# Kernel tuning notes

Hardware: AMD Instinct MI355X
Metric: run time of the kernel (lower is better)

The kernel has to match this reference:

```python
import jax, jax.numpy as jnp
import numpy as np

def setup_inputs() -> dict:
    key = jax.random.key(0)
    k1, k2 = jax.random.split(key)
    N, M, D = 4096, 4096, 1024
    set1 = jax.random.normal(k1, (N, D), dtype=jnp.float32)
    set2 = jax.random.normal(k2, (M, D), dtype=jnp.float32)
    return {"set1": set1, "set2": set2}

def _l2_dist(x, y):
    # mean over D of squared differences, computed via the expanded GEMM form
    D = x.shape[-1]
    x2 = jnp.sum(x * x, axis=-1)          # [N]
    y2 = jnp.sum(y * y, axis=-1)          # [M]
    xy = jnp.einsum('nd,md->nm', x, y)    # [N, M]
    return (x2[:, None] - 2.0 * xy + y2[None, :]) / D

def reference(set1, set2):
    dist = _l2_dist(set1, set2)                 # [N, M]
    t1 = jnp.mean(jnp.min(dist, axis=1))        # nearest set2 point per set1 point
    t2 = jnp.mean(jnp.min(dist, axis=0))        # nearest set1 point per set2 point
    return (t1 + t2) * 0.5
```

## Files before the change

### kernel.cpp

```cpp
#include <hip/hip_runtime.h>
#include <hip/hip_bf16.h>
#include <stdint.h>


#define NPTS 4096
#define MPTS 4096
#define DDIM 1024

typedef __attribute__((ext_vector_type(8))) short bf16x8;
typedef __attribute__((ext_vector_type(4))) float f32x4;

__device__ __forceinline__ unsigned short f2bf(float f) {
    unsigned int u = __float_as_uint(f);
    unsigned int r = 0x7FFFu + ((u >> 16) & 1u);
    return (unsigned short)((u + r) >> 16);
}

__device__ __forceinline__ void gl_lds16(const void* g, void* l) {
    __builtin_amdgcn_global_load_lds(
        (const __attribute__((address_space(1))) unsigned int*)g,
        (__attribute__((address_space(3))) unsigned int*)l, 16, 0, 0);
}

__global__ __launch_bounds__(256) void prepass_kernel(
    const float* __restrict__ s1, const float* __restrict__ s2,
    unsigned short* __restrict__ b1, unsigned short* __restrict__ b2,
    float* __restrict__ norms, unsigned int* __restrict__ mins) {
    const int row = blockIdx.x * 4 + (threadIdx.x >> 6);
    const int lane = threadIdx.x & 63;
    const float* src;
    unsigned short* dst;
    if (row < NPTS) { src = s1 + (size_t)row * DDIM; dst = b1 + (size_t)row * DDIM; }
    else            { src = s2 + (size_t)(row - NPTS) * DDIM; dst = b2 + (size_t)(row - NPTS) * DDIM; }
    float sq = 0.f;
    #pragma unroll
    for (int i = 0; i < 4; ++i) {
        float4 v = ((const float4*)src)[lane + i * 64];
        sq += v.x * v.x + v.y * v.y + v.z * v.z + v.w * v.w;
        ushort4 o;
        o.x = f2bf(v.x); o.y = f2bf(v.y); o.z = f2bf(v.z); o.w = f2bf(v.w);
        ((ushort4*)dst)[lane + i * 64] = o;
    }
    #pragma unroll
    for (int off = 32; off; off >>= 1) sq += __shfl_down(sq, off, 64);
    if (lane == 0) { norms[row] = sq; mins[row] = 0x7f7f7f7fu; }
}


#define STAGE_H(ldsBase, gRowBase, kcol) do {                                   \
    gl_lds16((gRowBase) + (size_t)(wave * 8 + srow) * DDIM + (kcol) + schoff,   \
             ldsb + (ldsBase) + wave * 1024);                                   \
    gl_lds16((gRowBase) + (size_t)(64 + wave * 8 + srow) * DDIM + (kcol) + schoff, \
             ldsb + (ldsBase) + 8192 + wave * 1024);                            \
} while (0)

#define RD_A(CURB, aq) do {                                                     \
    _Pragma("unroll")                                                           \
    for (int fl_ = 0; fl_ < 4; ++fl_) {                                         \
        const int row_ = wr * 128 + (aq) * 64 + fl_ * 16 + r0;                  \
        af[fl_][0] = *(const bf16x8*)(ldsb + (CURB) + row_ * 128 + ch0);        \
        af[fl_][1] = *(const bf16x8*)(ldsb + (CURB) + row_ * 128 + ch1);        \
    }                                                                           \
} while (0)

#define RD_B(CURB, bq, dst) do {                                                \
    _Pragma("unroll")                                                           \
    for (int fj_ = 0; fj_ < 2; ++fj_) {                                         \
        const int col_ = wc * 64 + (bq) * 32 + fj_ * 16 + r0;                   \
        dst[fj_][0] = *(const bf16x8*)(ldsb + (CURB) + 32768 + col_ * 128 + ch0); \
        dst[fj_][1] = *(const bf16x8*)(ldsb + (CURB) + 32768 + col_ * 128 + ch1); \
    }                                                                           \
} while (0)

#define MFMA_Q(aq, bq, BF)                                                      \
    _Pragma("unroll")                                                           \
    for (int fl_ = 0; fl_ < 4; ++fl_) {                                         \
        _Pragma("unroll")                                                       \
        for (int fj_ = 0; fj_ < 2; ++fj_) {                                     \
            acc[(aq) * 4 + fl_][(bq) * 2 + fj_] =                               \
                __builtin_amdgcn_mfma_f32_16x16x32_bf16(af[fl_][0], BF[fj_][0], \
                    acc[(aq) * 4 + fl_][(bq) * 2 + fj_], 0, 0, 0);              \
            acc[(aq) * 4 + fl_][(bq) * 2 + fj_] =                               \
                __builtin_amdgcn_mfma_f32_16x16x32_bf16(af[fl_][1], BF[fj_][1], \
                    acc[(aq) * 4 + fl_][(bq) * 2 + fj_], 0, 0, 0);              \
        }                                                                       \
    }

#define BARRIER_MFMA(aq, bq, BF, WAITSTMT) do {                                 \
    __builtin_amdgcn_s_barrier();                                               \
    asm volatile("s_waitcnt lgkmcnt(0)" ::: "memory");                          \
    __builtin_amdgcn_sched_barrier(0);                                          \
    __builtin_amdgcn_s_setprio(1);                                              \
    MFMA_Q(aq, bq, BF);                                                         \
    __builtin_amdgcn_s_setprio(0);                                              \
    WAITSTMT;                                                                   \
    __builtin_amdgcn_s_barrier();                                               \
} while (0)

#define TILE(t, CURB, NXTB) do {                                                \
    const int kN1_ = ((t) + 1) * 64, kN2_ = ((t) + 2) * 64;                     \
                                                 \
    RD_A(CURB, 0); RD_B(CURB, 0, bf0);                                          \
    if ((t) + 1 < 16) STAGE_H((NXTB) + 49152, Bb + 128 * DDIM, kN1_);           \
    BARRIER_MFMA(0, 0, bf0, );                                                  \
                                                 \
    RD_B(CURB, 1, bf1);                                                         \
    if ((t) + 1 < 16) STAGE_H((NXTB) + 16384, Ab + 128 * DDIM, kN1_);           \
    BARRIER_MFMA(0, 1, bf1, );                                                  \
                                                 \
    RD_A(CURB, 1);                                                              \
    if ((t) + 2 < 16) STAGE_H((CURB) + 32768, Bb, kN2_);                        \
    BARRIER_MFMA(1, 1, bf1, );                                                  \
                                   \
    if ((t) + 2 < 16) STAGE_H((CURB) + 0, Ab, kN2_);                            \
    BARRIER_MFMA(1, 0, bf0,                                                     \
        if ((t) < 14) { asm volatile("s_waitcnt vmcnt(4)" ::: "memory"); }      \
        else if ((t) == 14) { asm volatile("s_waitcnt vmcnt(0)" ::: "memory"); });\
} while (0)

__global__ __launch_bounds__(512, 2) void cham_gemm_kernel(
    const unsigned short* __restrict__ A,
    const unsigned short* __restrict__ B,
    const float* __restrict__ x2, const float* __restrict__ y2,
    unsigned int* __restrict__ rowmin, unsigned int* __restrict__ colmin) {
    __shared__ __align__(16) char lds[131072];
    char* ldsb = lds;

    const int bi = blockIdx.x & 15;
    const int bj = blockIdx.x >> 4;
    const int tid = threadIdx.x;
    const int wave = tid >> 6;
    const int lane = tid & 63;
    const int wr = wave >> 2;
    const int wc = wave & 3;
    const int r0 = lane & 15;
    const int q = lane >> 4;

    const int ch0 = ((q ^ (r0 & 7)) << 4);
    const int ch1 = (((4 + q) ^ (r0 & 7)) << 4);

    const int srow = lane >> 3;
    const int schoff = (((lane & 7) ^ srow) * 8);

    const unsigned short* Ab = A + (size_t)(bi * 256) * DDIM;
    const unsigned short* Bb = B + (size_t)(bj * 256) * DDIM;

    f32x4 acc[8][4];
    #pragma unroll
    for (int i = 0; i < 8; ++i)
        #pragma unroll
        for (int j = 0; j < 4; ++j)
            acc[i][j] = (f32x4){0.f, 0.f, 0.f, 0.f};

    bf16x8 af[4][2], bf0[2][2], bf1[2][2];

    STAGE_H(0 + 32768, Bb, 0);
    STAGE_H(0 + 0, Ab, 0);
    STAGE_H(0 + 49152, Bb + 128 * DDIM, 0);
    STAGE_H(0 + 16384, Ab + 128 * DDIM, 0);
    STAGE_H(65536 + 32768, Bb, 64);
    STAGE_H(65536 + 0, Ab, 64);
    asm volatile("s_waitcnt vmcnt(4)" ::: "memory");
    __builtin_amdgcn_s_barrier();

    for (int tt = 0; tt < 8; ++tt) {
        const int te = 2 * tt, to = 2 * tt + 1;
        TILE(te, 0, 65536);
        TILE(to, 65536, 0);
    }

    const float invD = 1.0f / (float)DDIM;
    const int nb = bi * 256 + wr * 128;
    const int mb = bj * 256 + wc * 64;

    float y2v[4];
    #pragma unroll
    for (int fj = 0; fj < 4; ++fj)
        y2v[fj] = y2[mb + (fj >> 1) * 32 + (fj & 1) * 16 + r0];

    float cv[4];
    #pragma unroll
    for (int fj = 0; fj < 4; ++fj) cv[fj] = 3.0e38f;

    #pragma unroll
    for (int fi = 0; fi < 8; ++fi) {
        #pragma unroll
        for (int rg = 0; rg < 4; ++rg) {
            const int n = nb + fi * 16 + q * 4 + rg;
            const float x2v = x2[n];
            float rv = 3.0e38f;
            #pragma unroll
            for (int fj = 0; fj < 4; ++fj) {
                float d = (x2v + y2v[fj] - 2.0f * acc[fi][fj][rg]) * invD;
                rv = fminf(rv, d);
                cv[fj] = fminf(cv[fj], d);
            }
            rv = fminf(rv, __shfl_xor(rv, 1, 64));
            rv = fminf(rv, __shfl_xor(rv, 2, 64));
            rv = fminf(rv, __shfl_xor(rv, 4, 64));
            rv = fminf(rv, __shfl_xor(rv, 8, 64));
            if (r0 == 0) atomicMin(&rowmin[n], __float_as_uint(rv));
        }
    }

    #pragma unroll
    for (int fj = 0; fj < 4; ++fj) {
        float v = cv[fj];
        v = fminf(v, __shfl_xor(v, 16, 64));
        v = fminf(v, __shfl_xor(v, 32, 64));
        if (lane < 16)
            atomicMin(&colmin[mb + (fj >> 1) * 32 + (fj & 1) * 16 + lane],
                      __float_as_uint(v));
    }
}

__global__ __launch_bounds__(1024) void finredux_kernel(
    const unsigned int* __restrict__ mins , float* __restrict__ out) {
    int t = threadIdx.x;
    float s = 0.f;
    #pragma unroll
    for (int i = 0; i < 8; ++i) s += __uint_as_float(mins[t + i * 1024]);
    #pragma unroll
    for (int off = 32; off; off >>= 1) s += __shfl_down(s, off, 64);
    __shared__ float ws_[16];
    if ((t & 63) == 0) ws_[t >> 6] = s;
    __syncthreads();
    if (t == 0) {
        float tot = 0.f;
        #pragma unroll
        for (int i = 0; i < 16; ++i) tot += ws_[i];
        out[0] = tot * (1.0f / 8192.0f);
    }
}

extern "C" void kernel_launch(void* const* d_in, const int* in_sizes, int n_in,
                              void* d_out, int out_size, void* d_ws, size_t ws_size,
                              hipStream_t stream) {
    const float* s1 = (const float*)d_in[0];
    const float* s2 = (const float*)d_in[1];
    char* ws = (char*)d_ws;

    unsigned short* b1 = (unsigned short*)ws;
    unsigned short* b2 = (unsigned short*)(ws + 8388608);
    float* norms       = (float*)(ws + 16777216);
    unsigned int* mins = (unsigned int*)(ws + 16777216 + 32768);
    float* out = (float*)d_out;

    prepass_kernel<<<2048, 256, 0, stream>>>(s1, s2, b1, b2, norms, mins);
    cham_gemm_kernel<<<256, 512, 0, stream>>>(b1, b2, norms, norms + NPTS,
                                              mins, mins + NPTS);
    finredux_kernel<<<1, 1024, 0, stream>>>(mins, out);
}
```

Before: 123.8 us.

## Fuse final reduction into GEMM via last-block counter and remap blocks per XCD

Removes the separate final reduction kernel. The last GEMM block to finish, found through an atomic counter that the prepass resets, now sums the min array and writes the output. Blocks are also remapped so each XCD gets a compact 4x8 group of tiles for better L2 reuse. The prepass stores its bf16 outputs with nontemporal stores. The changes aim to cut one launch and improve cache locality, at the cost of an extra fence and atomic in every GEMM block.

New measurement: 153.3 us. 23.9% more time.

```diff
diff --git a/kernel.cpp b/kernel.cpp
--- a/kernel.cpp
+++ b/kernel.cpp
@@ -9,6 +9,7 @@
 
 typedef __attribute__((ext_vector_type(8))) short bf16x8;
 typedef __attribute__((ext_vector_type(4))) float f32x4;
+typedef __attribute__((ext_vector_type(4))) unsigned short us4;
 
 __device__ __forceinline__ unsigned short f2bf(float f) {
     unsigned int u = __float_as_uint(f);
@@ -25,9 +26,11 @@
 __global__ __launch_bounds__(256) void prepass_kernel(
     const float* __restrict__ s1, const float* __restrict__ s2,
     unsigned short* __restrict__ b1, unsigned short* __restrict__ b2,
-    float* __restrict__ norms, unsigned int* __restrict__ mins) {
+    float* __restrict__ norms, unsigned int* __restrict__ mins,
+    unsigned int* __restrict__ ctr) {
     const int row = blockIdx.x * 4 + (threadIdx.x >> 6);
     const int lane = threadIdx.x & 63;
+    if (blockIdx.x == 0 && threadIdx.x == 0) ctr[0] = 0u;
     const float* src;
     unsigned short* dst;
     if (row < NPTS) { src = s1 + (size_t)row * DDIM; dst = b1 + (size_t)row * DDIM; }
@@ -37,9 +40,9 @@
     for (int i = 0; i < 4; ++i) {
         float4 v = ((const float4*)src)[lane + i * 64];
         sq += v.x * v.x + v.y * v.y + v.z * v.z + v.w * v.w;
-        ushort4 o;
+        us4 o;
         o.x = f2bf(v.x); o.y = f2bf(v.y); o.z = f2bf(v.z); o.w = f2bf(v.w);
-        ((ushort4*)dst)[lane + i * 64] = o;
+        __builtin_nontemporal_store(o, ((us4*)dst) + lane + i * 64);
     }
     #pragma unroll
     for (int off = 32; off; off >>= 1) sq += __shfl_down(sq, off, 64);
@@ -99,19 +102,15 @@
 
 #define TILE(t, CURB, NXTB) do {                                                \
     const int kN1_ = ((t) + 1) * 64, kN2_ = ((t) + 2) * 64;                     \
-                                                 \
     RD_A(CURB, 0); RD_B(CURB, 0, bf0);                                          \
     if ((t) + 1 < 16) STAGE_H((NXTB) + 49152, Bb + 128 * DDIM, kN1_);           \
     BARRIER_MFMA(0, 0, bf0, );                                                  \
-                                                 \
     RD_B(CURB, 1, bf1);                                                         \
     if ((t) + 1 < 16) STAGE_H((NXTB) + 16384, Ab + 128 * DDIM, kN1_);           \
     BARRIER_MFMA(0, 1, bf1, );                                                  \
-                                                 \
     RD_A(CURB, 1);                                                              \
     if ((t) + 2 < 16) STAGE_H((CURB) + 32768, Bb, kN2_);                        \
     BARRIER_MFMA(1, 1, bf1, );                                                  \
-                                   \
     if ((t) + 2 < 16) STAGE_H((CURB) + 0, Ab, kN2_);                            \
     BARRIER_MFMA(1, 0, bf0,                                                     \
         if ((t) < 14) { asm volatile("s_waitcnt vmcnt(4)" ::: "memory"); }      \
@@ -122,12 +121,19 @@
     const unsigned short* __restrict__ A,
     const unsigned short* __restrict__ B,
     const float* __restrict__ x2, const float* __restrict__ y2,
-    unsigned int* __restrict__ rowmin, unsigned int* __restrict__ colmin) {
+    unsigned int* __restrict__ mins,
+    unsigned int* __restrict__ ctr, float* __restrict__ out) {
     __shared__ __align__(16) char lds[131072];
     char* ldsb = lds;
-
-    const int bi = blockIdx.x & 15;
-    const int bj = blockIdx.x >> 4;
+    unsigned int* rowmin = mins;
+    unsigned int* colmin = mins + NPTS;
+
+    const int g = blockIdx.x;
+    const int xcd = g & 7;
+    const int s = g >> 3;
+    const int bi = (xcd >> 1) * 4 + (s >> 3);
+    const int bj = (xcd & 1) * 8 + (s & 7);
+
     const int tid = threadIdx.x;
     const int wave = tid >> 6;
     const int lane = tid & 63;
@@ -138,7 +144,6 @@
 
     const int ch0 = ((q ^ (r0 & 7)) << 4);
     const int ch1 = (((4 + q) ^ (r0 & 7)) << 4);
-
     const int srow = lane >> 3;
     const int schoff = (((lane & 7) ^ srow) * 8);
 
@@ -212,24 +217,29 @@
             atomicMin(&colmin[mb + (fj >> 1) * 32 + (fj & 1) * 16 + lane],
                       __float_as_uint(v));
     }
-}
-
-__global__ __launch_bounds__(1024) void finredux_kernel(
-    const unsigned int* __restrict__ mins , float* __restrict__ out) {
-    int t = threadIdx.x;
-    float s = 0.f;
-    #pragma unroll
-    for (int i = 0; i < 8; ++i) s += __uint_as_float(mins[t + i * 1024]);
-    #pragma unroll
-    for (int off = 32; off; off >>= 1) s += __shfl_down(s, off, 64);
-    __shared__ float ws_[16];
-    if ((t & 63) == 0) ws_[t >> 6] = s;
+
+    __threadfence();
     __syncthreads();
-    if (t == 0) {
-        float tot = 0.f;
-        #pragma unroll
-        for (int i = 0; i < 16; ++i) tot += ws_[i];
-        out[0] = tot * (1.0f / 8192.0f);
+    volatile unsigned int* flag = (volatile unsigned int*)ldsb;
+    if (tid == 0) flag[0] = atomicAdd(ctr, 1u);
+    __syncthreads();
+    if (flag[0] == 255u) {
+        __threadfence();
+        float sum = 0.f;
+        #pragma unroll
+        for (int i = 0; i < 16; ++i)
+            sum += __uint_as_float(mins[tid + i * 512]);
+        #pragma unroll
+        for (int off = 32; off; off >>= 1) sum += __shfl_down(sum, off, 64);
+        float* red = (float*)(ldsb + 64);
+        if (lane == 0) red[wave] = sum;
+        __syncthreads();
+        if (tid == 0) {
+            float tot = 0.f;
+            #pragma unroll
+            for (int i = 0; i < 8; ++i) tot += red[i];
+            out[0] = tot * (1.0f / 8192.0f);
+        }
     }
 }
 
@@ -244,10 +254,10 @@
     unsigned short* b2 = (unsigned short*)(ws + 8388608);
     float* norms       = (float*)(ws + 16777216);
     unsigned int* mins = (unsigned int*)(ws + 16777216 + 32768);
+    unsigned int* ctr  = (unsigned int*)(ws + 16777216 + 65536);
     float* out = (float*)d_out;
 
-    prepass_kernel<<<2048, 256, 0, stream>>>(s1, s2, b1, b2, norms, mins);
+    prepass_kernel<<<2048, 256, 0, stream>>>(s1, s2, b1, b2, norms, mins, ctr);
     cham_gemm_kernel<<<256, 512, 0, stream>>>(b1, b2, norms, norms + NPTS,
-                                              mins, mins + NPTS);
-    finredux_kernel<<<1, 1024, 0, stream>>>(mins, out);
-}
+                                              mins, ctr, out);
+}
```
